# Performance work log

Measured on AMD Instinct MI355X. Metric: run time of the kernel, lower is better.

Reference implementation:

```python
import jax, jax.numpy as jnp
import numpy as np

EPS = 1e-15
CLAMP = 1e-7


def _sqnorm(x):
    return jnp.sum(x * x, axis=-1, keepdims=True)


def _norm(x):
    return jnp.sqrt(jnp.maximum(_sqnorm(x), EPS))


def artanh(x):
    x = jnp.clip(x, -1.0 + CLAMP, 1.0 - CLAMP)
    return 0.5 * (jnp.log1p(x) - jnp.log1p(-x))


def expmap0(u):
    # Poincare ball, c = 1: exp map at origin
    n = _norm(u)
    return jnp.tanh(n) * u / n


def logmap0(p):
    n = _norm(p)
    return artanh(n) * p / n


def mobius_add(x, y):
    x2 = _sqnorm(x)
    y2 = _sqnorm(y)
    xy = jnp.sum(x * y, axis=-1, keepdims=True)
    num = (1.0 + 2.0 * xy + y2) * x + (1.0 - x2) * y
    den = 1.0 + 2.0 * xy + x2 * y2
    return num / jnp.maximum(den, EPS)


def expmap(u, p):
    # exp map of tangent u at ball point p
    n = _norm(u)
    lam = 2.0 / jnp.maximum(1.0 - _sqnorm(p), EPS)
    second = jnp.tanh(0.5 * lam * n) * u / n
    return mobius_add(p, second)


def ptransp0(x, u):
    # parallel transport of tangent u from origin to x: u * (lambda_0 / lambda_x)
    return u * (1.0 - _sqnorm(x))


def setup_inputs() -> dict:
    key = jax.random.key(0)
    k1, k2, k3, k4, k5, k6 = jax.random.split(key, 6)
    n_slot, n_int, d = 30000, 20000, 128
    n_edges, n_rel = 640000, 16
    n_nodes = n_slot + n_int
    return {
        "slot_embed": 0.05 * jax.random.normal(k1, (n_slot, d), dtype=jnp.float32),
        "int_embed": 0.05 * jax.random.normal(k2, (n_int, d), dtype=jnp.float32),
        "relation_embed": 0.05 * jax.random.normal(k3, (n_rel, d), dtype=jnp.float32),
        "src": jax.random.randint(k4, (n_edges,), 0, n_nodes, dtype=jnp.int64) if jax.config.jax_enable_x64 else jax.random.randint(k4, (n_edges,), 0, n_nodes, dtype=jnp.int32),
        "dst": jax.random.randint(k5, (n_edges,), 0, n_nodes, dtype=jnp.int32),
        "edge_type": jax.random.randint(k6, (n_edges,), 0, n_rel, dtype=jnp.int32),
    }


def reference(slot_embed, int_embed, relation_embed, src, dst, edge_type):
    n_slot = slot_embed.shape[0]
    n_nodes = n_slot + int_embed.shape[0]
    embed = jnp.concatenate([slot_embed, int_embed], axis=0)   # 'node'
    node1 = expmap0(embed)                                     # 'node1'

    # per-edge hyperbolic transform: gather src/dst/relation rows
    src_p = node1[src]                          # [E, d] point on ball
    tangent = embed[dst] + relation_embed[edge_type]  # [E, d] tangent at origin
    tan_sum = logmap0(expmap(ptransp0(src_p, tangent), src_p))  # [E, d]

    # g_inv reverses edges, so copy_e + mean aggregates onto original SRC nodes
    sums = jax.ops.segment_sum(tan_sum, src, num_segments=n_nodes)
    cnts = jax.ops.segment_sum(jnp.ones((src.shape[0],), tan_sum.dtype), src,
                               num_segments=n_nodes)
    out = sums / jnp.maximum(cnts, 1.0)[:, None]  # isolated nodes -> 0 (DGL mean)
    return out[:n_slot], out[n_slot:]
```

## Files before the change

### kernel.cpp

```cpp
#include <hip/hip_runtime.h>
#include <math.h>

#define EPSF 1e-15f
#define CLAMPF 1e-7f
#define D 128
#define ELLW 64
#define MAXREL 16

typedef float v2f __attribute__((ext_vector_type(2)));

__device__ __forceinline__ float rcpf(float x) { return __builtin_amdgcn_rcpf(x); }
__device__ __forceinline__ float rsqf(float x) { return __builtin_amdgcn_rsqf(x); }

__device__ __forceinline__ v2f vfma2(v2f a, v2f b, v2f c) {
#if __has_builtin(__builtin_elementwise_fma)
    return __builtin_elementwise_fma(a, b, c);
#else
    v2f r; r.x = fmaf(a.x, b.x, c.x); r.y = fmaf(a.y, b.y, c.y); return r;
#endif
}

__device__ __forceinline__ float tanh_fast2(float z2) {
    float e2 = __expf(z2);
    return 1.0f - 2.0f * rcpf(e2 + 1.0f);
}

template<int CTRL>
__device__ __forceinline__ float dpp_add(float v) {
    int s = __builtin_bit_cast(int, v);
    int m = __builtin_amdgcn_update_dpp(s, s, CTRL, 0xF, 0xF, false);
    return v + __builtin_bit_cast(float, m);
}
__device__ __forceinline__ float red16(float v) {
    v = dpp_add<0x128>(v);
    v = dpp_add<0x124>(v);
    v = dpp_add<0x122>(v);
    v = dpp_add<0x121>(v);
    return v;
}

struct v2x2 { v2f lo, hi; };
__device__ __forceinline__ v2x2 ld8(const float* p) {
    float4 f = *(const float4*)p;
    v2x2 r; r.lo = (v2f){f.x, f.y}; r.hi = (v2f){f.z, f.w}; return r;
}

__global__ void build_ell_kernel(const int* __restrict__ src,
                                 const int* __restrict__ dst,
                                 const int* __restrict__ etype,
                                 int* __restrict__ cnt,
                                 int* __restrict__ ell, int n_edges) {
    int i = blockIdx.x * blockDim.x + threadIdx.x;
    int base = i * 4;
    if (base >= n_edges) return;
    if (base + 4 <= n_edges) {
        int4 s = *(const int4*)(src + base);
        int4 d = *(const int4*)(dst + base);
        int4 e = *(const int4*)(etype + base);
        int p;
        p = atomicAdd(cnt + s.x, 1); if (p < ELLW) ell[s.x * ELLW + p] = d.x | (e.x << 20);
        p = atomicAdd(cnt + s.y, 1); if (p < ELLW) ell[s.y * ELLW + p] = d.y | (e.y << 20);
        p = atomicAdd(cnt + s.z, 1); if (p < ELLW) ell[s.z * ELLW + p] = d.z | (e.z << 20);
        p = atomicAdd(cnt + s.w, 1); if (p < ELLW) ell[s.w * ELLW + p] = d.w | (e.w << 20);
    } else {
        for (int k = base; k < n_edges; ++k) {
            int p = atomicAdd(cnt + src[k], 1);
            if (p < ELLW) ell[src[k] * ELLW + p] = dst[k] | (etype[k] << 20);
        }
    }
}

__global__ __launch_bounds__(256)
void node_agg_kernel(const float* __restrict__ slot,
                     const float* __restrict__ intm_virt,
                     const float* __restrict__ rel,
                     const int* __restrict__ ell,
                     const int* __restrict__ cnt,
                     float* __restrict__ out,
                     int n_slot, int n_nodes, int n_rel) {
    __shared__ __align__(16) float rel_lds[MAXREL * D];
    {
        const float4* rs = (const float4*)rel;
        float4* rd = (float4*)rel_lds;
        int tot = n_rel * (D / 4);
        for (int i = threadIdx.x; i < tot; i += 256) rd[i] = rs[i];
    }
    __syncthreads();

    int wid  = (blockIdx.x * blockDim.x + threadIdx.x) >> 6;
    int lane = threadIdx.x & 63;
    if (wid >= n_nodes) return;
    int sl = lane & 15;
    int g  = lane >> 4;

    const float* xrow = ((wid < n_slot) ? slot : intm_virt) + (size_t)wid * D + sl * 8;
    v2x2 ea = ld8(xrow);
    v2x2 eb = ld8(xrow + 4);
    v2f ssv = ea.lo * ea.lo;
    ssv = vfma2(ea.hi, ea.hi, ssv);
    ssv = vfma2(eb.lo, eb.lo, ssv);
    ssv = vfma2(eb.hi, eb.hi, ssv);
    float ss = red16(ssv.x + ssv.y);

    float irn = rsqf(fmaxf(ss, EPSF));
    float n   = ss * irn;
    float thn = tanh_fast2(2.0f * n);
    float tf  = thn * irn;
    float x2  = thn * thn;
    v2f tfv = (v2f){tf, tf};
    v2f x0 = ea.lo * tfv, x1 = ea.hi * tfv;
    v2f x2v_ = eb.lo * tfv, x3 = eb.hi * tfv;

    float fac  = 1.0f - x2;
    float fac2 = fac * fac;

    int cn = cnt[wid];
    int m  = (cn < ELLW) ? cn : ELLW;
    const int* erow = ell + (size_t)wid * ELLW;

    int pk_all = (lane < m) ? erow[lane] : 0;

    float accx = 0.0f;
    v2f ac0 = (v2f){0.f, 0.f}, ac1 = ac0, ac2 = ac0, ac3 = ac0;

    for (int p = 0; p < m; p += 4) {
        int ep = p + g;
        bool ok = ep < m;
        int pk = __shfl(pk_all, ep & 63, 64);
        unsigned di = (unsigned)pk & 0xFFFFF;
        unsigned ri = ((unsigned)pk) >> 20;

        const float* drow = (((int)di < n_slot) ? slot : intm_virt)
                            + (size_t)di * D + sl * 8;
        const float* rl = rel_lds + ri * D + sl * 8;
        v2x2 dv0 = ld8(drow);
        v2x2 dv1 = ld8(drow + 4);
        v2x2 rv0 = ld8(rl);
        v2x2 rv1 = ld8(rl + 4);

        v2f t0 = dv0.lo + rv0.lo;
        v2f t1 = dv0.hi + rv0.hi;
        v2f t2 = dv1.lo + rv1.lo;
        v2f t3 = dv1.hi + rv1.hi;

        v2f ttv = t0 * t0;
        ttv = vfma2(t1, t1, ttv);
        ttv = vfma2(t2, t2, ttv);
        ttv = vfma2(t3, t3, ttv);
        v2f xtv = x0 * t0;
        xtv = vfma2(x1, t1, xtv);
        xtv = vfma2(x2v_, t2, xtv);
        xtv = vfma2(x3, t3, xtv);

        float tt = red16(ttv.x + ttv.y);
        float xt = red16(xtv.x + xtv.y);

        float irt = rsqf(fmaxf(tt, EPSF));
        float st2 = 2.0f * tt * irt;
        float th  = tanh_fast2(st2);
        float w   = th * irt;
        float y2  = th * th;
        float xy  = w * xt;
        float two_xy = xy + xy;
        float opx = 1.0f + two_xy;
        float a   = opx + y2;
        float den = fmaf(x2, y2, opx);
        float invden = rcpf(fmaxf(den, EPSF));
        float poly = fmaf(a * a, x2, fmaf(a * fac, two_xy, fac2 * y2));
        float qq   = invden * invden * poly;
        float irq  = rsqf(fmaxf(qq, EPSF));
        float nq   = qq * irq;
        float cl   = fminf(nq, 1.0f - CLAMPF);
        float at   = 0.5f * __logf((1.0f + cl) * rcpf(1.0f - cl));
        float sc2  = at * irq;
        float k    = sc2 * invden;
        float cx   = k * a;
        float ct   = k * w * fac;
        if (!ok) { cx = 0.0f; ct = 0.0f; }

        accx += cx;
        v2f ctv = (v2f){ct, ct};
        ac0 = vfma2(ctv, t0, ac0);
        ac1 = vfma2(ctv, t1, ac1);
        ac2 = vfma2(ctv, t2, ac2);
        ac3 = vfma2(ctv, t3, ac3);
    }

    v2f axv = (v2f){accx, accx};
    ac0 = vfma2(axv, x0, ac0);
    ac1 = vfma2(axv, x1, ac1);
    ac2 = vfma2(axv, x2v_, ac2);
    ac3 = vfma2(axv, x3, ac3);

    float v0 = ac0.x, v1 = ac0.y, v2 = ac1.x, v3 = ac1.y;
    float v4 = ac2.x, v5 = ac2.y, v6 = ac3.x, v7 = ac3.y;
    #pragma unroll
    for (int d = 16; d < 64; d <<= 1) {
        v0 += __shfl_xor(v0, d, 64);
        v1 += __shfl_xor(v1, d, 64);
        v2 += __shfl_xor(v2, d, 64);
        v3 += __shfl_xor(v3, d, 64);
        v4 += __shfl_xor(v4, d, 64);
        v5 += __shfl_xor(v5, d, 64);
        v6 += __shfl_xor(v6, d, 64);
        v7 += __shfl_xor(v7, d, 64);
    }

    if (lane < 16) {
        float invcnt = rcpf(fmaxf((float)cn, 1.0f));
        float4 w0 = make_float4(v0 * invcnt, v1 * invcnt, v2 * invcnt, v3 * invcnt);
        float4 w1 = make_float4(v4 * invcnt, v5 * invcnt, v6 * invcnt, v7 * invcnt);
        float* orow = out + (size_t)wid * D + sl * 8;
        *(float4*)(orow)     = w0;
        *(float4*)(orow + 4) = w1;
    }
}

extern "C" void kernel_launch(void* const* d_in, const int* in_sizes, int n_in,
                              void* d_out, int out_size, void* d_ws, size_t ws_size,
                              hipStream_t stream) {
    const float* slot = (const float*)d_in[0];
    const float* intm = (const float*)d_in[1];
    const float* rel  = (const float*)d_in[2];
    const int*   src  = (const int*)d_in[3];
    const int*   dst  = (const int*)d_in[4];
    const int*   etyp = (const int*)d_in[5];

    int n_slot  = in_sizes[0] / D;
    int n_int   = in_sizes[1] / D;
    int n_rel   = in_sizes[2] / D;
    int n_nodes = n_slot + n_int;
    int n_edges = in_sizes[3];

    float* out = (float*)d_out;
    const float* intm_virt = intm - (size_t)n_slot * D;

    int* cnt = (int*)d_ws;
    int* ell = cnt + n_nodes;

    hipMemsetAsync(cnt, 0, (size_t)n_nodes * sizeof(int), stream);

    {
        int threads = 256;
        int nthreads = (n_edges + 3) / 4;
        int blocks = (nthreads + threads - 1) / threads;
        build_ell_kernel<<<blocks, threads, 0, stream>>>(src, dst, etyp, cnt, ell,
                                                         n_edges);
    }
    {
        int threads = 256;
        int blocks = (n_nodes * 64 + threads - 1) / threads;
        node_agg_kernel<<<blocks, threads, 0, stream>>>(slot, intm_virt, rel, ell,
                                                        cnt, out, n_slot, n_nodes,
                                                        n_rel);
    }
}
```

Before: 93.82 us.

## Process eight edges per wave with 8-lane rows and read relations from global

Result: slower. 127.5 us (+35.8%).

```diff
diff --git a/kernel.cpp b/kernel.cpp
--- a/kernel.cpp
+++ b/kernel.cpp
@@ -5,7 +5,6 @@
 #define CLAMPF 1e-7f
 #define D 128
 #define ELLW 64
-#define MAXREL 16
 
 typedef float v2f __attribute__((ext_vector_type(2)));
 
@@ -31,18 +30,11 @@
     int m = __builtin_amdgcn_update_dpp(s, s, CTRL, 0xF, 0xF, false);
     return v + __builtin_bit_cast(float, m);
 }
-__device__ __forceinline__ float red16(float v) {
-    v = dpp_add<0x128>(v);
-    v = dpp_add<0x124>(v);
-    v = dpp_add<0x122>(v);
-    v = dpp_add<0x121>(v);
+__device__ __forceinline__ float red8(float v) {
+    v = dpp_add<0xB1>(v);
+    v = dpp_add<0x4E>(v);
+    v = dpp_add<0x141>(v);
     return v;
-}
-
-struct v2x2 { v2f lo, hi; };
-__device__ __forceinline__ v2x2 ld8(const float* p) {
-    float4 f = *(const float4*)p;
-    v2x2 r; r.lo = (v2f){f.x, f.y}; r.hi = (v2f){f.z, f.w}; return r;
 }
 
 __global__ void build_ell_kernel(const int* __restrict__ src,
@@ -77,30 +69,29 @@
                      const int* __restrict__ ell,
                      const int* __restrict__ cnt,
                      float* __restrict__ out,
-                     int n_slot, int n_nodes, int n_rel) {
-    __shared__ __align__(16) float rel_lds[MAXREL * D];
-    {
-        const float4* rs = (const float4*)rel;
-        float4* rd = (float4*)rel_lds;
-        int tot = n_rel * (D / 4);
-        for (int i = threadIdx.x; i < tot; i += 256) rd[i] = rs[i];
-    }
-    __syncthreads();
-
+                     int n_slot, int n_nodes) {
     int wid  = (blockIdx.x * blockDim.x + threadIdx.x) >> 6;
     int lane = threadIdx.x & 63;
     if (wid >= n_nodes) return;
-    int sl = lane & 15;
-    int g  = lane >> 4;
-
-    const float* xrow = ((wid < n_slot) ? slot : intm_virt) + (size_t)wid * D + sl * 8;
-    v2x2 ea = ld8(xrow);
-    v2x2 eb = ld8(xrow + 4);
-    v2f ssv = ea.lo * ea.lo;
-    ssv = vfma2(ea.hi, ea.hi, ssv);
-    ssv = vfma2(eb.lo, eb.lo, ssv);
-    ssv = vfma2(eb.hi, eb.hi, ssv);
-    float ss = red16(ssv.x + ssv.y);
+    int sl = lane & 7;
+    int g  = lane >> 3;
+
+    const float* xrow = ((wid < n_slot) ? slot : intm_virt) + (size_t)wid * D + sl * 16;
+    v2f x[8];
+    {
+        float4 f0 = ((const float4*)xrow)[0];
+        float4 f1 = ((const float4*)xrow)[1];
+        float4 f2 = ((const float4*)xrow)[2];
+        float4 f3 = ((const float4*)xrow)[3];
+        x[0] = (v2f){f0.x, f0.y}; x[1] = (v2f){f0.z, f0.w};
+        x[2] = (v2f){f1.x, f1.y}; x[3] = (v2f){f1.z, f1.w};
+        x[4] = (v2f){f2.x, f2.y}; x[5] = (v2f){f2.z, f2.w};
+        x[6] = (v2f){f3.x, f3.y}; x[7] = (v2f){f3.z, f3.w};
+    }
+    v2f ssv = x[0] * x[0];
+    #pragma unroll
+    for (int i = 1; i < 8; ++i) ssv = vfma2(x[i], x[i], ssv);
+    float ss = red8(ssv.x + ssv.y);
 
     float irn = rsqf(fmaxf(ss, EPSF));
     float n   = ss * irn;
@@ -108,52 +99,62 @@
     float tf  = thn * irn;
     float x2  = thn * thn;
     v2f tfv = (v2f){tf, tf};
-    v2f x0 = ea.lo * tfv, x1 = ea.hi * tfv;
-    v2f x2v_ = eb.lo * tfv, x3 = eb.hi * tfv;
+    #pragma unroll
+    for (int i = 0; i < 8; ++i) x[i] *= tfv;
 
     float fac  = 1.0f - x2;
     float fac2 = fac * fac;
 
     int cn = cnt[wid];
     int m  = (cn < ELLW) ? cn : ELLW;
+
     const int* erow = ell + (size_t)wid * ELLW;
-
     int pk_all = (lane < m) ? erow[lane] : 0;
 
     float accx = 0.0f;
-    v2f ac0 = (v2f){0.f, 0.f}, ac1 = ac0, ac2 = ac0, ac3 = ac0;
-
-    for (int p = 0; p < m; p += 4) {
+    v2f acc[8];
+    #pragma unroll
+    for (int i = 0; i < 8; ++i) acc[i] = (v2f){0.f, 0.f};
+
+    for (int p = 0; p < m; p += 8) {
         int ep = p + g;
         bool ok = ep < m;
-        int pk = __shfl(pk_all, ep & 63, 64);
+        int pk = __shfl(pk_all, ep, 64);
         unsigned di = (unsigned)pk & 0xFFFFF;
         unsigned ri = ((unsigned)pk) >> 20;
 
         const float* drow = (((int)di < n_slot) ? slot : intm_virt)
-                            + (size_t)di * D + sl * 8;
-        const float* rl = rel_lds + ri * D + sl * 8;
-        v2x2 dv0 = ld8(drow);
-        v2x2 dv1 = ld8(drow + 4);
-        v2x2 rv0 = ld8(rl);
-        v2x2 rv1 = ld8(rl + 4);
-
-        v2f t0 = dv0.lo + rv0.lo;
-        v2f t1 = dv0.hi + rv0.hi;
-        v2f t2 = dv1.lo + rv1.lo;
-        v2f t3 = dv1.hi + rv1.hi;
-
-        v2f ttv = t0 * t0;
-        ttv = vfma2(t1, t1, ttv);
-        ttv = vfma2(t2, t2, ttv);
-        ttv = vfma2(t3, t3, ttv);
-        v2f xtv = x0 * t0;
-        xtv = vfma2(x1, t1, xtv);
-        xtv = vfma2(x2v_, t2, xtv);
-        xtv = vfma2(x3, t3, xtv);
-
-        float tt = red16(ttv.x + ttv.y);
-        float xt = red16(xtv.x + xtv.y);
+                            + (size_t)di * D + sl * 16;
+        const float* rrow = rel + (size_t)ri * D + sl * 16;
+
+        float4 d0 = ((const float4*)drow)[0];
+        float4 d1 = ((const float4*)drow)[1];
+        float4 d2 = ((const float4*)drow)[2];
+        float4 d3 = ((const float4*)drow)[3];
+        float4 r0 = ((const float4*)rrow)[0];
+        float4 r1 = ((const float4*)rrow)[1];
+        float4 r2 = ((const float4*)rrow)[2];
+        float4 r3 = ((const float4*)rrow)[3];
+
+        v2f t[8];
+        t[0] = (v2f){d0.x + r0.x, d0.y + r0.y};
+        t[1] = (v2f){d0.z + r0.z, d0.w + r0.w};
+        t[2] = (v2f){d1.x + r1.x, d1.y + r1.y};
+        t[3] = (v2f){d1.z + r1.z, d1.w + r1.w};
+        t[4] = (v2f){d2.x + r2.x, d2.y + r2.y};
+        t[5] = (v2f){d2.z + r2.z, d2.w + r2.w};
+        t[6] = (v2f){d3.x + r3.x, d3.y + r3.y};
+        t[7] = (v2f){d3.z + r3.z, d3.w + r3.w};
+
+        v2f ttv = t[0] * t[0];
+        v2f xtv = x[0] * t[0];
+        #pragma unroll
+        for (int i = 1; i < 8; ++i) {
+            ttv = vfma2(t[i], t[i], ttv);
+            xtv = vfma2(x[i], t[i], xtv);
+        }
+        float tt = red8(ttv.x + ttv.y);
+        float xt = red8(xtv.x + xtv.y);
 
         float irt = rsqf(fmaxf(tt, EPSF));
         float st2 = 2.0f * tt * irt;
@@ -180,39 +181,34 @@
 
         accx += cx;
         v2f ctv = (v2f){ct, ct};
-        ac0 = vfma2(ctv, t0, ac0);
-        ac1 = vfma2(ctv, t1, ac1);
-        ac2 = vfma2(ctv, t2, ac2);
-        ac3 = vfma2(ctv, t3, ac3);
+        #pragma unroll
+        for (int i = 0; i < 8; ++i) acc[i] = vfma2(ctv, t[i], acc[i]);
     }
 
     v2f axv = (v2f){accx, accx};
-    ac0 = vfma2(axv, x0, ac0);
-    ac1 = vfma2(axv, x1, ac1);
-    ac2 = vfma2(axv, x2v_, ac2);
-    ac3 = vfma2(axv, x3, ac3);
-
-    float v0 = ac0.x, v1 = ac0.y, v2 = ac1.x, v3 = ac1.y;
-    float v4 = ac2.x, v5 = ac2.y, v6 = ac3.x, v7 = ac3.y;
-    #pragma unroll
-    for (int d = 16; d < 64; d <<= 1) {
-        v0 += __shfl_xor(v0, d, 64);
-        v1 += __shfl_xor(v1, d, 64);
-        v2 += __shfl_xor(v2, d, 64);
-        v3 += __shfl_xor(v3, d, 64);
-        v4 += __shfl_xor(v4, d, 64);
-        v5 += __shfl_xor(v5, d, 64);
-        v6 += __shfl_xor(v6, d, 64);
-        v7 += __shfl_xor(v7, d, 64);
-    }
-
-    if (lane < 16) {
+    #pragma unroll
+    for (int i = 0; i < 8; ++i) acc[i] = vfma2(axv, x[i], acc[i]);
+
+    float v[16];
+    #pragma unroll
+    for (int i = 0; i < 8; ++i) { v[2*i] = acc[i].x; v[2*i+1] = acc[i].y; }
+    #pragma unroll
+    for (int d = 8; d < 64; d <<= 1) {
+        #pragma unroll
+        for (int j = 0; j < 16; ++j) v[j] += __shfl_xor(v[j], d, 64);
+    }
+
+    if (lane < 8) {
         float invcnt = rcpf(fmaxf((float)cn, 1.0f));
-        float4 w0 = make_float4(v0 * invcnt, v1 * invcnt, v2 * invcnt, v3 * invcnt);
-        float4 w1 = make_float4(v4 * invcnt, v5 * invcnt, v6 * invcnt, v7 * invcnt);
-        float* orow = out + (size_t)wid * D + sl * 8;
-        *(float4*)(orow)     = w0;
-        *(float4*)(orow + 4) = w1;
+        float* orow = out + (size_t)wid * D + sl * 16;
+        float4 w0 = make_float4(v[0]*invcnt,  v[1]*invcnt,  v[2]*invcnt,  v[3]*invcnt);
+        float4 w1 = make_float4(v[4]*invcnt,  v[5]*invcnt,  v[6]*invcnt,  v[7]*invcnt);
+        float4 w2 = make_float4(v[8]*invcnt,  v[9]*invcnt,  v[10]*invcnt, v[11]*invcnt);
+        float4 w3 = make_float4(v[12]*invcnt, v[13]*invcnt, v[14]*invcnt, v[15]*invcnt);
+        ((float4*)orow)[0] = w0;
+        ((float4*)orow)[1] = w1;
+        ((float4*)orow)[2] = w2;
+        ((float4*)orow)[3] = w3;
     }
 }
 
@@ -228,7 +224,6 @@
 
     int n_slot  = in_sizes[0] / D;
     int n_int   = in_sizes[1] / D;
-    int n_rel   = in_sizes[2] / D;
     int n_nodes = n_slot + n_int;
     int n_edges = in_sizes[3];
 
@@ -251,7 +246,6 @@
         int threads = 256;
         int blocks = (n_nodes * 64 + threads - 1) / threads;
         node_agg_kernel<<<blocks, threads, 0, stream>>>(slot, intm_virt, rel, ell,
-                                                        cnt, out, n_slot, n_nodes,
-                                                        n_rel);
-    }
-}
+                                                        cnt, out, n_slot, n_nodes);
+    }
+}
```

## Process two edges per group per iteration and read relations from global memory

Applied to the files above, without the earlier changes.

Result: slower. 100.6 us (+7.3%).

```diff
diff --git a/kernel.cpp b/kernel.cpp
--- a/kernel.cpp
+++ b/kernel.cpp
@@ -5,7 +5,6 @@
 #define CLAMPF 1e-7f
 #define D 128
 #define ELLW 64
-#define MAXREL 16
 
 typedef float v2f __attribute__((ext_vector_type(2)));
 
@@ -77,16 +76,7 @@
                      const int* __restrict__ ell,
                      const int* __restrict__ cnt,
                      float* __restrict__ out,
-                     int n_slot, int n_nodes, int n_rel) {
-    __shared__ __align__(16) float rel_lds[MAXREL * D];
-    {
-        const float4* rs = (const float4*)rel;
-        float4* rd = (float4*)rel_lds;
-        int tot = n_rel * (D / 4);
-        for (int i = threadIdx.x; i < tot; i += 256) rd[i] = rs[i];
-    }
-    __syncthreads();
-
+                     int n_slot, int n_nodes) {
     int wid  = (blockIdx.x * blockDim.x + threadIdx.x) >> 6;
     int lane = threadIdx.x & 63;
     if (wid >= n_nodes) return;
@@ -123,67 +113,114 @@
     float accx = 0.0f;
     v2f ac0 = (v2f){0.f, 0.f}, ac1 = ac0, ac2 = ac0, ac3 = ac0;
 
-    for (int p = 0; p < m; p += 4) {
-        int ep = p + g;
-        bool ok = ep < m;
-        int pk = __shfl(pk_all, ep & 63, 64);
-        unsigned di = (unsigned)pk & 0xFFFFF;
-        unsigned ri = ((unsigned)pk) >> 20;
-
-        const float* drow = (((int)di < n_slot) ? slot : intm_virt)
-                            + (size_t)di * D + sl * 8;
-        const float* rl = rel_lds + ri * D + sl * 8;
-        v2x2 dv0 = ld8(drow);
-        v2x2 dv1 = ld8(drow + 4);
-        v2x2 rv0 = ld8(rl);
-        v2x2 rv1 = ld8(rl + 4);
-
-        v2f t0 = dv0.lo + rv0.lo;
-        v2f t1 = dv0.hi + rv0.hi;
-        v2f t2 = dv1.lo + rv1.lo;
-        v2f t3 = dv1.hi + rv1.hi;
-
-        v2f ttv = t0 * t0;
-        ttv = vfma2(t1, t1, ttv);
-        ttv = vfma2(t2, t2, ttv);
-        ttv = vfma2(t3, t3, ttv);
-        v2f xtv = x0 * t0;
-        xtv = vfma2(x1, t1, xtv);
-        xtv = vfma2(x2v_, t2, xtv);
-        xtv = vfma2(x3, t3, xtv);
-
-        float tt = red16(ttv.x + ttv.y);
-        float xt = red16(xtv.x + xtv.y);
-
-        float irt = rsqf(fmaxf(tt, EPSF));
-        float st2 = 2.0f * tt * irt;
-        float th  = tanh_fast2(st2);
-        float w   = th * irt;
-        float y2  = th * th;
-        float xy  = w * xt;
-        float two_xy = xy + xy;
-        float opx = 1.0f + two_xy;
-        float a   = opx + y2;
-        float den = fmaf(x2, y2, opx);
-        float invden = rcpf(fmaxf(den, EPSF));
-        float poly = fmaf(a * a, x2, fmaf(a * fac, two_xy, fac2 * y2));
-        float qq   = invden * invden * poly;
-        float irq  = rsqf(fmaxf(qq, EPSF));
-        float nq   = qq * irq;
-        float cl   = fminf(nq, 1.0f - CLAMPF);
-        float at   = 0.5f * __logf((1.0f + cl) * rcpf(1.0f - cl));
-        float sc2  = at * irq;
-        float k    = sc2 * invden;
-        float cx   = k * a;
-        float ct   = k * w * fac;
-        if (!ok) { cx = 0.0f; ct = 0.0f; }
-
-        accx += cx;
-        v2f ctv = (v2f){ct, ct};
-        ac0 = vfma2(ctv, t0, ac0);
-        ac1 = vfma2(ctv, t1, ac1);
-        ac2 = vfma2(ctv, t2, ac2);
-        ac3 = vfma2(ctv, t3, ac3);
+    for (int p = 0; p < m; p += 8) {
+        int ep0 = p + g;
+        int ep1 = p + 4 + g;
+        bool ok0 = ep0 < m;
+        bool ok1 = ep1 < m;
+        int pk0 = __shfl(pk_all, ep0 & 63, 64);
+        int pk1 = __shfl(pk_all, ep1 & 63, 64);
+        unsigned di0 = (unsigned)pk0 & 0xFFFFF, ri0 = ((unsigned)pk0) >> 20;
+        unsigned di1 = (unsigned)pk1 & 0xFFFFF, ri1 = ((unsigned)pk1) >> 20;
+
+        const float* drow0 = (((int)di0 < n_slot) ? slot : intm_virt)
+                             + (size_t)di0 * D + sl * 8;
+        const float* drow1 = (((int)di1 < n_slot) ? slot : intm_virt)
+                             + (size_t)di1 * D + sl * 8;
+        const float* rrow0 = rel + (size_t)ri0 * D + sl * 8;
+        const float* rrow1 = rel + (size_t)ri1 * D + sl * 8;
+
+        v2x2 dA0 = ld8(drow0);
+        v2x2 dB0 = ld8(drow0 + 4);
+        v2x2 dA1 = ld8(drow1);
+        v2x2 dB1 = ld8(drow1 + 4);
+        v2x2 rA0 = ld8(rrow0);
+        v2x2 rB0 = ld8(rrow0 + 4);
+        v2x2 rA1 = ld8(rrow1);
+        v2x2 rB1 = ld8(rrow1 + 4);
+
+        v2f s0 = dA0.lo + rA0.lo;
+        v2f s1 = dA0.hi + rA0.hi;
+        v2f s2 = dB0.lo + rB0.lo;
+        v2f s3 = dB0.hi + rB0.hi;
+        v2f u0 = dA1.lo + rA1.lo;
+        v2f u1 = dA1.hi + rA1.hi;
+        v2f u2 = dB1.lo + rB1.lo;
+        v2f u3 = dB1.hi + rB1.hi;
+
+        v2f ttv0 = s0 * s0;
+        ttv0 = vfma2(s1, s1, ttv0);
+        ttv0 = vfma2(s2, s2, ttv0);
+        ttv0 = vfma2(s3, s3, ttv0);
+        v2f xtv0 = x0 * s0;
+        xtv0 = vfma2(x1, s1, xtv0);
+        xtv0 = vfma2(x2v_, s2, xtv0);
+        xtv0 = vfma2(x3, s3, xtv0);
+
+        v2f ttv1 = u0 * u0;
+        ttv1 = vfma2(u1, u1, ttv1);
+        ttv1 = vfma2(u2, u2, ttv1);
+        ttv1 = vfma2(u3, u3, ttv1);
+        v2f xtv1 = x0 * u0;
+        xtv1 = vfma2(x1, u1, xtv1);
+        xtv1 = vfma2(x2v_, u2, xtv1);
+        xtv1 = vfma2(x3, u3, xtv1);
+
+        float tt0 = red16(ttv0.x + ttv0.y);
+        float xt0 = red16(xtv0.x + xtv0.y);
+        float tt1 = red16(ttv1.x + ttv1.y);
+        float xt1 = red16(xtv1.x + xtv1.y);
+
+        float irt0 = rsqf(fmaxf(tt0, EPSF));
+        float irt1 = rsqf(fmaxf(tt1, EPSF));
+        float th0  = tanh_fast2(2.0f * tt0 * irt0);
+        float th1  = tanh_fast2(2.0f * tt1 * irt1);
+        float w0   = th0 * irt0;
+        float w1   = th1 * irt1;
+        float y20  = th0 * th0;
+        float y21  = th1 * th1;
+        float xy0  = w0 * xt0;
+        float xy1  = w1 * xt1;
+        float txy0 = xy0 + xy0;
+        float txy1 = xy1 + xy1;
+        float opx0 = 1.0f + txy0;
+        float opx1 = 1.0f + txy1;
+        float a0   = opx0 + y20;
+        float a1   = opx1 + y21;
+        float den0 = fmaf(x2, y20, opx0);
+        float den1 = fmaf(x2, y21, opx1);
+        float ivd0 = rcpf(fmaxf(den0, EPSF));
+        float ivd1 = rcpf(fmaxf(den1, EPSF));
+        float pl0  = fmaf(a0 * a0, x2, fmaf(a0 * fac, txy0, fac2 * y20));
+        float pl1  = fmaf(a1 * a1, x2, fmaf(a1 * fac, txy1, fac2 * y21));
+        float qq0  = ivd0 * ivd0 * pl0;
+        float qq1  = ivd1 * ivd1 * pl1;
+        float irq0 = rsqf(fmaxf(qq0, EPSF));
+        float irq1 = rsqf(fmaxf(qq1, EPSF));
+        float nq0  = qq0 * irq0;
+        float nq1  = qq1 * irq1;
+        float cl0  = fminf(nq0, 1.0f - CLAMPF);
+        float cl1  = fminf(nq1, 1.0f - CLAMPF);
+        float at0  = 0.5f * __logf((1.0f + cl0) * rcpf(1.0f - cl0));
+        float at1  = 0.5f * __logf((1.0f + cl1) * rcpf(1.0f - cl1));
+        float sA0  = at0 * irq0;
+        float sA1  = at1 * irq1;
+        float k0   = sA0 * ivd0;
+        float k1   = sA1 * ivd1;
+        float cx0  = k0 * a0;
+        float cx1  = k1 * a1;
+        float ct0  = k0 * w0 * fac;
+        float ct1  = k1 * w1 * fac;
+        if (!ok0) { cx0 = 0.0f; ct0 = 0.0f; }
+        if (!ok1) { cx1 = 0.0f; ct1 = 0.0f; }
+
+        accx += cx0 + cx1;
+        v2f c0 = (v2f){ct0, ct0};
+        v2f c1 = (v2f){ct1, ct1};
+        ac0 = vfma2(c0, s0, ac0); ac0 = vfma2(c1, u0, ac0);
+        ac1 = vfma2(c0, s1, ac1); ac1 = vfma2(c1, u1, ac1);
+        ac2 = vfma2(c0, s2, ac2); ac2 = vfma2(c1, u2, ac2);
+        ac3 = vfma2(c0, s3, ac3); ac3 = vfma2(c1, u3, ac3);
     }
 
     v2f axv = (v2f){accx, accx};
@@ -228,7 +265,6 @@
 
     int n_slot  = in_sizes[0] / D;
     int n_int   = in_sizes[1] / D;
-    int n_rel   = in_sizes[2] / D;
     int n_nodes = n_slot + n_int;
     int n_edges = in_sizes[3];
 
@@ -251,7 +287,6 @@
         int threads = 256;
         int blocks = (n_nodes * 64 + threads - 1) / threads;
         node_agg_kernel<<<blocks, threads, 0, stream>>>(slot, intm_virt, rel, ell,
-                                                        cnt, out, n_slot, n_nodes,
-                                                        n_rel);
-    }
-}
+                                                        cnt, out, n_slot, n_nodes);
+    }
+}
```

## Prefetch next edge rows in node aggregation loop and drop relation LDS staging

Applied to the files above, without the earlier changes.

Result: no change. 94.58 us (+0.8%).

```diff
diff --git a/kernel.cpp b/kernel.cpp
--- a/kernel.cpp
+++ b/kernel.cpp
@@ -5,12 +5,15 @@
 #define CLAMPF 1e-7f
 #define D 128
 #define ELLW 64
-#define MAXREL 16
+#define LOG2E2 2.885390081777927f
+#define HALF_LN2 0.34657359027997264f
 
 typedef float v2f __attribute__((ext_vector_type(2)));
 
 __device__ __forceinline__ float rcpf(float x) { return __builtin_amdgcn_rcpf(x); }
 __device__ __forceinline__ float rsqf(float x) { return __builtin_amdgcn_rsqf(x); }
+__device__ __forceinline__ float exp2h(float x) { return __builtin_amdgcn_exp2f(x); }
+__device__ __forceinline__ float log2h(float x) { return __builtin_amdgcn_logf(x); }
 
 __device__ __forceinline__ v2f vfma2(v2f a, v2f b, v2f c) {
 #if __has_builtin(__builtin_elementwise_fma)
@@ -20,8 +23,8 @@
 #endif
 }
 
-__device__ __forceinline__ float tanh_fast2(float z2) {
-    float e2 = __expf(z2);
+__device__ __forceinline__ float tanh_exp2(float zl) {
+    float e2 = exp2h(zl);
     return 1.0f - 2.0f * rcpf(e2 + 1.0f);
 }
 
@@ -77,16 +80,7 @@
                      const int* __restrict__ ell,
                      const int* __restrict__ cnt,
                      float* __restrict__ out,
-                     int n_slot, int n_nodes, int n_rel) {
-    __shared__ __align__(16) float rel_lds[MAXREL * D];
-    {
-        const float4* rs = (const float4*)rel;
-        float4* rd = (float4*)rel_lds;
-        int tot = n_rel * (D / 4);
-        for (int i = threadIdx.x; i < tot; i += 256) rd[i] = rs[i];
-    }
-    __syncthreads();
-
+                     int n_slot, int n_nodes) {
     int wid  = (blockIdx.x * blockDim.x + threadIdx.x) >> 6;
     int lane = threadIdx.x & 63;
     if (wid >= n_nodes) return;
@@ -103,8 +97,7 @@
     float ss = red16(ssv.x + ssv.y);
 
     float irn = rsqf(fmaxf(ss, EPSF));
-    float n   = ss * irn;
-    float thn = tanh_fast2(2.0f * n);
+    float thn = tanh_exp2(LOG2E2 * ss * irn);
     float tf  = thn * irn;
     float x2  = thn * thn;
     v2f tfv = (v2f){tf, tf};
@@ -123,67 +116,76 @@
     float accx = 0.0f;
     v2f ac0 = (v2f){0.f, 0.f}, ac1 = ac0, ac2 = ac0, ac3 = ac0;
 
-    for (int p = 0; p < m; p += 4) {
-        int ep = p + g;
-        bool ok = ep < m;
-        int pk = __shfl(pk_all, ep & 63, 64);
+    if (m > 0) {
+        int pk = __shfl(pk_all, g, 64);
         unsigned di = (unsigned)pk & 0xFFFFF;
         unsigned ri = ((unsigned)pk) >> 20;
-
         const float* drow = (((int)di < n_slot) ? slot : intm_virt)
                             + (size_t)di * D + sl * 8;
-        const float* rl = rel_lds + ri * D + sl * 8;
-        v2x2 dv0 = ld8(drow);
-        v2x2 dv1 = ld8(drow + 4);
-        v2x2 rv0 = ld8(rl);
-        v2x2 rv1 = ld8(rl + 4);
-
-        v2f t0 = dv0.lo + rv0.lo;
-        v2f t1 = dv0.hi + rv0.hi;
-        v2f t2 = dv1.lo + rv1.lo;
-        v2f t3 = dv1.hi + rv1.hi;
-
-        v2f ttv = t0 * t0;
-        ttv = vfma2(t1, t1, ttv);
-        ttv = vfma2(t2, t2, ttv);
-        ttv = vfma2(t3, t3, ttv);
-        v2f xtv = x0 * t0;
-        xtv = vfma2(x1, t1, xtv);
-        xtv = vfma2(x2v_, t2, xtv);
-        xtv = vfma2(x3, t3, xtv);
-
-        float tt = red16(ttv.x + ttv.y);
-        float xt = red16(xtv.x + xtv.y);
-
-        float irt = rsqf(fmaxf(tt, EPSF));
-        float st2 = 2.0f * tt * irt;
-        float th  = tanh_fast2(st2);
-        float w   = th * irt;
-        float y2  = th * th;
-        float xy  = w * xt;
-        float two_xy = xy + xy;
-        float opx = 1.0f + two_xy;
-        float a   = opx + y2;
-        float den = fmaf(x2, y2, opx);
-        float invden = rcpf(fmaxf(den, EPSF));
-        float poly = fmaf(a * a, x2, fmaf(a * fac, two_xy, fac2 * y2));
-        float qq   = invden * invden * poly;
-        float irq  = rsqf(fmaxf(qq, EPSF));
-        float nq   = qq * irq;
-        float cl   = fminf(nq, 1.0f - CLAMPF);
-        float at   = 0.5f * __logf((1.0f + cl) * rcpf(1.0f - cl));
-        float sc2  = at * irq;
-        float k    = sc2 * invden;
-        float cx   = k * a;
-        float ct   = k * w * fac;
-        if (!ok) { cx = 0.0f; ct = 0.0f; }
-
-        accx += cx;
-        v2f ctv = (v2f){ct, ct};
-        ac0 = vfma2(ctv, t0, ac0);
-        ac1 = vfma2(ctv, t1, ac1);
-        ac2 = vfma2(ctv, t2, ac2);
-        ac3 = vfma2(ctv, t3, ac3);
+        const float* rrow = rel + (size_t)ri * D + sl * 8;
+        v2x2 dA = ld8(drow), dB = ld8(drow + 4);
+        v2x2 rA = ld8(rrow), rB = ld8(rrow + 4);
+
+        for (int p = 0; p < m; p += 4) {
+            bool ok = (p + g) < m;
+
+            v2f t0 = dA.lo + rA.lo;
+            v2f t1 = dA.hi + rA.hi;
+            v2f t2 = dB.lo + rB.lo;
+            v2f t3 = dB.hi + rB.hi;
+
+            v2f ttv = t0 * t0;
+            ttv = vfma2(t1, t1, ttv);
+            ttv = vfma2(t2, t2, ttv);
+            ttv = vfma2(t3, t3, ttv);
+            v2f xtv = x0 * t0;
+            xtv = vfma2(x1, t1, xtv);
+            xtv = vfma2(x2v_, t2, xtv);
+            xtv = vfma2(x3, t3, xtv);
+
+            float tt = red16(ttv.x + ttv.y);
+            float xt = red16(xtv.x + xtv.y);
+
+            if (p + 4 < m) {
+                int pk2 = __shfl(pk_all, (p + 4 + g) & 63, 64);
+                unsigned di2 = (unsigned)pk2 & 0xFFFFF;
+                unsigned ri2 = ((unsigned)pk2) >> 20;
+                const float* drow2 = (((int)di2 < n_slot) ? slot : intm_virt)
+                                     + (size_t)di2 * D + sl * 8;
+                const float* rrow2 = rel + (size_t)ri2 * D + sl * 8;
+                dA = ld8(drow2); dB = ld8(drow2 + 4);
+                rA = ld8(rrow2); rB = ld8(rrow2 + 4);
+            }
+
+            float irt = rsqf(fmaxf(tt, EPSF));
+            float th  = tanh_exp2(LOG2E2 * tt * irt);
+            float w   = th * irt;
+            float y2  = th * th;
+            float xy  = w * xt;
+            float two_xy = xy + xy;
+            float opx = 1.0f + two_xy;
+            float a   = opx + y2;
+            float den = fmaf(x2, y2, opx);
+            float invden = rcpf(fmaxf(den, EPSF));
+            float poly = fmaf(a * a, x2, fmaf(a * fac, two_xy, fac2 * y2));
+            float qq   = invden * invden * poly;
+            float irq  = rsqf(fmaxf(qq, EPSF));
+            float nq   = qq * irq;
+            float cl   = fminf(nq, 1.0f - CLAMPF);
+            float at   = HALF_LN2 * log2h((1.0f + cl) * rcpf(1.0f - cl));
+            float sc2  = at * irq;
+            float k    = sc2 * invden;
+            float cx   = k * a;
+            float ct   = k * w * fac;
+            if (!ok) { cx = 0.0f; ct = 0.0f; }
+
+            accx += cx;
+            v2f ctv = (v2f){ct, ct};
+            ac0 = vfma2(ctv, t0, ac0);
+            ac1 = vfma2(ctv, t1, ac1);
+            ac2 = vfma2(ctv, t2, ac2);
+            ac3 = vfma2(ctv, t3, ac3);
+        }
     }
 
     v2f axv = (v2f){accx, accx};
@@ -228,7 +230,6 @@
 
     int n_slot  = in_sizes[0] / D;
     int n_int   = in_sizes[1] / D;
-    int n_rel   = in_sizes[2] / D;
     int n_nodes = n_slot + n_int;
     int n_edges = in_sizes[3];
 
@@ -238,7 +239,7 @@
     int* cnt = (int*)d_ws;
     int* ell = cnt + n_nodes;
 
-    hipMemsetAsync(cnt, 0, (size_t)n_nodes * sizeof(int), stream);
+    (void)hipMemsetAsync(cnt, 0, (size_t)n_nodes * sizeof(int), stream);
 
     {
         int threads = 256;
@@ -251,7 +252,6 @@
         int threads = 256;
         int blocks = (n_nodes * 64 + threads - 1) / threads;
         node_agg_kernel<<<blocks, threads, 0, stream>>>(slot, intm_virt, rel, ell,
-                                                        cnt, out, n_slot, n_nodes,
-                                                        n_rel);
-    }
-}
+                                                        cnt, out, n_slot, n_nodes);
+    }
+}
```
